# Kernel optimization log

Hardware: AMD Instinct MI355X
Metric: run time of the kernel (lower is better)

Reference implementation:

```python
import jax, jax.numpy as jnp
import numpy as np

HIDDEN = 256
HORIZON = 24
FMET = 16
OUT = 1
EPS = 1e-5


def setup_inputs() -> dict:
    key = jax.random.key(0)
    ks = jax.random.split(key, 12)
    B, N = 16, 1000
    final_h = jax.random.normal(ks[0], (B, N, HIDDEN), dtype=jnp.float32)
    future_met = jax.random.normal(ks[1], (B, HORIZON, N, FMET), dtype=jnp.float32)
    # step_queries: xavier_uniform over (max_horizon, hidden)
    lim_q = float(np.sqrt(6.0 / (HORIZON + HIDDEN)))
    step_queries = jax.random.uniform(ks[2], (HORIZON, HIDDEN), minval=-lim_q, maxval=lim_q, dtype=jnp.float32)
    # future_met_proj: Linear(FMET -> HIDDEN); store weight as (FMET, HIDDEN)
    lim_fm = float(np.sqrt(1.0 / FMET))
    W_fm = jax.random.uniform(ks[3], (FMET, HIDDEN), minval=-lim_fm, maxval=lim_fm, dtype=jnp.float32)
    b_fm = jax.random.uniform(ks[4], (HIDDEN,), minval=-lim_fm, maxval=lim_fm, dtype=jnp.float32)
    gamma = jnp.ones((HIDDEN,), dtype=jnp.float32)
    beta = jnp.zeros((HIDDEN,), dtype=jnp.float32)
    lim1 = float(np.sqrt(1.0 / HIDDEN))
    W1 = jax.random.uniform(ks[5], (HIDDEN, HIDDEN), minval=-lim1, maxval=lim1, dtype=jnp.float32)
    b1 = jax.random.uniform(ks[6], (HIDDEN,), minval=-lim1, maxval=lim1, dtype=jnp.float32)
    W2 = jax.random.uniform(ks[7], (HIDDEN, OUT), minval=-lim1, maxval=lim1, dtype=jnp.float32)
    b2 = jax.random.uniform(ks[8], (OUT,), minval=-lim1, maxval=lim1, dtype=jnp.float32)
    return {
        "final_h": final_h,
        "future_met": future_met,
        "step_queries": step_queries,
        "W_fm": W_fm,
        "b_fm": b_fm,
        "gamma": gamma,
        "beta": beta,
        "W1": W1,
        "b1": b1,
        "W2": W2,
        "b2": b2,
    }


def _layer_norm(x, gamma, beta):
    mu = jnp.mean(x, axis=-1, keepdims=True)
    var = jnp.mean(jnp.square(x - mu), axis=-1, keepdims=True)
    return (x - mu) * jax.lax.rsqrt(var + EPS) * gamma + beta


def reference(final_h, future_met, step_queries, W_fm, b_fm, gamma, beta, W1, b1, W2, b2):
    # final_h: (B, N, H); future_met: (B, T, N, F)
    # combined: (B, N, T, H) = broadcast(final_h) + queries + proj(future_met)
    combined = final_h[:, :, None, :] + step_queries[None, None, :, :]
    fm = jnp.transpose(future_met, (0, 2, 1, 3))  # (B, N, T, F)
    combined = combined + (jnp.einsum("bntf,fh->bnth", fm, W_fm) + b_fm)
    x = _layer_norm(combined, gamma, beta)
    x = jax.nn.gelu(x @ W1 + b1, approximate=False)
    # dropout is identity in eval mode
    out = x @ W2 + b2  # (B, N, T, OUT)
    return jnp.transpose(out, (0, 2, 1, 3))  # (B, T, N, OUT)
```

## Files before the change

### kernel.cpp

```cpp
#include <hip/hip_runtime.h>
#include <hip/hip_bf16.h>
#include <stdint.h>

#define MROWS 32
#define LDA   264
#define FMS   40

typedef __bf16 bf16x8 __attribute__((ext_vector_type(8)));
typedef float  f32x4  __attribute__((ext_vector_type(4)));

__device__ __forceinline__ unsigned short f2bf(float f) {
    union { float f; uint32_t u; } v; v.f = f;
    return (unsigned short)((v.u + 0x7FFFu + ((v.u >> 16) & 1u)) >> 16);
}

__device__ __forceinline__ ushort2 pk_bf16(float a, float b) {
    union { __hip_bfloat162 v; ushort2 u; } c;
    c.v = __float22bfloat162_rn(make_float2(a, b));
    return c.u;
}

__device__ __forceinline__ float gelu_fast(float v) {
    const float t = v * v;
    const float p = fmaf(0.044715f, t, 1.0f);
    const float u = v * p;
    const float e = __builtin_amdgcn_exp2f(u * -2.3021131160186336f);
    return v * __builtin_amdgcn_rcpf(1.0f + e);
}

__global__ __launch_bounds__(256) void prep(const float* __restrict__ W1,
                                            const float* __restrict__ step_q,
                                            const float* __restrict__ b_fm,
                                            const float* __restrict__ W_fm,
                                            unsigned short* __restrict__ w1frag,
                                            float* __restrict__ sqb,
                                            unsigned short* __restrict__ wfmfrag) {
    const int blk = blockIdx.x, tid = threadIdx.x;
    if (blk < 256) {
        const int o  = blk * 256 + tid;
        const int e  = o & 7;
        const int l  = (o >> 3) & 63;
        const int fr = o >> 9;
        const int kk = fr & 7, j = (fr >> 3) & 3, w = fr >> 5;
        const int col = l & 15, qr = l >> 4;
        const int n = (w << 6) + (j << 4) + col;
        const int k = (kk << 5) + (qr << 3) + e;
        w1frag[o] = f2bf(W1[(k << 8) + n]);
    } else if (blk == 256) {
        const float bv = b_fm[tid];
        #pragma unroll
        for (int t = 0; t < 24; ++t) sqb[t * 256 + tid] = step_q[t * 256 + tid] + bv;
    } else {
        #pragma unroll
        for (int f = 0; f < 4; ++f) {
            const int fr = (f << 8) + tid;
            const int l = fr & 63, j = (fr >> 6) & 3, w = fr >> 8;
            const int col = l & 15, qr = l >> 4;
            const int n = (w << 6) + (j << 4) + col;
            #pragma unroll
            for (int e = 0; e < 8; ++e) {
                const int k = (qr << 3) + e;
                wfmfrag[(fr << 3) + e] = (k < 16) ? f2bf(W_fm[(k << 8) + n]) : (unsigned short)0;
            }
        }
    }
}

__global__ __launch_bounds__(256, 6) void fused_head(
    const float* __restrict__ final_h, const float* __restrict__ future_met,
    const float* __restrict__ gamma,   const float* __restrict__ beta,
    const float* __restrict__ b1,      const float* __restrict__ W2,
    const float* __restrict__ b2,      const unsigned short* __restrict__ w1frag,
    const float* __restrict__ sqb,     const unsigned short* __restrict__ wfmfrag,
    float* __restrict__ out)
{
    __shared__ __align__(16) unsigned short Abuf[MROWS * LDA];
    __shared__ __align__(16) unsigned short fmA[MROWS * FMS];
    __shared__ float2 red[4][MROWS];
    __shared__ float2 mv[MROWS];
    __shared__ float  part[4][MROWS];

    const int tid = threadIdx.x;
    const int w   = tid >> 6;
    const int l   = tid & 63;
    const int col = l & 15;
    const int qr  = l >> 4;
    const int m0  = blockIdx.x * MROWS;

    if (tid < 128) {
        const int row = tid >> 2, f0 = (tid & 3) << 2;
        const int m  = m0 + row;
        const int bn = m / 24, tt = m - bn * 24;
        const int b  = bn / 1000, n = bn - b * 1000;
        const float4 v = *(const float4*)&future_met[((((b * 24 + tt) * 1000) + n) << 4) + f0];
        ushort2 lo = pk_bf16(v.x, v.y), hi = pk_bf16(v.z, v.w);
        ushort4 o; o.x = lo.x; o.y = lo.y; o.z = hi.x; o.w = hi.y;
        *(ushort4*)&fmA[row * FMS + f0] = o;
    }
    {
        const int row = tid >> 3, k = 16 + ((tid & 7) << 1);
        *(unsigned int*)&fmA[row * FMS + k] = 0u;
    }
    __syncthreads();

    f32x4 acc[2][4];
    #pragma unroll
    for (int i = 0; i < 2; ++i) {
        #pragma unroll
        for (int r = 0; r < 4; ++r) {
            const int m  = (i << 4) + (qr << 2) + r;
            const int mm = m0 + m;
            const int bn = mm / 24, tt = mm - bn * 24;
            const float* fh = final_h + (bn << 8) + (w << 6) + col;
            const float* sb = sqb + (tt << 8) + (w << 6) + col;
            #pragma unroll
            for (int j = 0; j < 4; ++j)
                acc[i][j][r] = fh[j << 4] + sb[j << 4];
        }
    }
    {
        const bf16x8 af0 = *(const bf16x8*)&fmA[col * FMS + (qr << 3)];
        const bf16x8 af1 = *(const bf16x8*)&fmA[(16 + col) * FMS + (qr << 3)];
        const unsigned short* Bwf = wfmfrag + (w << 11) + (l << 3);
        #pragma unroll
        for (int j = 0; j < 4; ++j) {
            const bf16x8 bf = *(const bf16x8*)(Bwf + (j << 9));
            acc[0][j] = __builtin_amdgcn_mfma_f32_16x16x32_bf16(af0, bf, acc[0][j], 0, 0, 0);
            acc[1][j] = __builtin_amdgcn_mfma_f32_16x16x32_bf16(af1, bf, acc[1][j], 0, 0, 0);
        }
    }

    #pragma unroll
    for (int i = 0; i < 2; ++i) {
        #pragma unroll
        for (int r = 0; r < 4; ++r) {
            float s = 0.f, q = 0.f;
            #pragma unroll
            for (int j = 0; j < 4; ++j) { const float v = acc[i][j][r]; s += v; q = fmaf(v, v, q); }
            s += __shfl_xor(s, 1); q += __shfl_xor(q, 1);
            s += __shfl_xor(s, 2); q += __shfl_xor(q, 2);
            s += __shfl_xor(s, 4); q += __shfl_xor(q, 4);
            s += __shfl_xor(s, 8); q += __shfl_xor(q, 8);
            if (col == 0) red[w][(i << 4) + (qr << 2) + r] = make_float2(s, q);
        }
    }
    __syncthreads();
    if (tid < MROWS) {
        const float2 a0 = red[0][tid], a1 = red[1][tid], a2 = red[2][tid], a3 = red[3][tid];
        const float S = a0.x + a1.x + a2.x + a3.x;
        const float Q = a0.y + a1.y + a2.y + a3.y;
        const float mu = S * 0.00390625f;
        const float rstd = rsqrtf(Q * 0.00390625f - mu * mu + 1e-5f);
        mv[tid] = make_float2(mu, rstd);
    }
    __syncthreads();

    #pragma unroll
    for (int i = 0; i < 2; ++i) {
        #pragma unroll
        for (int r = 0; r < 4; ++r) {
            const int m = (i << 4) + (qr << 2) + r;
            const float2 p = mv[m];
            float vj[4];
            #pragma unroll
            for (int j = 0; j < 4; ++j) {
                const int n = (w << 6) + (j << 4) + col;
                const float s1 = p.y * gamma[n];
                const float s2 = fmaf(-p.x, s1, beta[n]);
                vj[j] = fmaf(acc[i][j][r], s1, s2);
            }
            const ushort2 p01 = pk_bf16(vj[0], vj[1]);
            const ushort2 p23 = pk_bf16(vj[2], vj[3]);
            unsigned short* Ab = &Abuf[m * LDA + (w << 6) + col];
            Ab[0]  = p01.x; Ab[16] = p01.y;
            Ab[32] = p23.x; Ab[48] = p23.y;
        }
    }
    __syncthreads();

    #pragma unroll
    for (int i = 0; i < 2; ++i)
        #pragma unroll
        for (int j = 0; j < 4; ++j)
            acc[i][j] = (f32x4){0.f, 0.f, 0.f, 0.f};

    {
        const unsigned short* Bw  = w1frag + (w << 14) + (l << 3);
        const unsigned short* Ab0 = &Abuf[col * LDA + (qr << 3)];
        const unsigned short* Ab1 = &Abuf[(16 + col) * LDA + (qr << 3)];
        #pragma unroll
        for (int kk = 0; kk < 8; ++kk) {
            const bf16x8 a0 = *(const bf16x8*)(Ab0 + (kk << 5));
            const bf16x8 a1 = *(const bf16x8*)(Ab1 + (kk << 5));
            #pragma unroll
            for (int j = 0; j < 4; ++j) {
                const bf16x8 bf = *(const bf16x8*)(Bw + (j << 12) + (kk << 9));
                acc[0][j] = __builtin_amdgcn_mfma_f32_16x16x32_bf16(a0, bf, acc[0][j], 0, 0, 0);
                acc[1][j] = __builtin_amdgcn_mfma_f32_16x16x32_bf16(a1, bf, acc[1][j], 0, 0, 0);
            }
        }
    }

    {
        float b1v[4], w2v[4];
        #pragma unroll
        for (int j = 0; j < 4; ++j) {
            const int n = (w << 6) + (j << 4) + col;
            b1v[j] = b1[n]; w2v[j] = W2[n];
        }
        #pragma unroll
        for (int i = 0; i < 2; ++i) {
            #pragma unroll
            for (int r = 0; r < 4; ++r) {
                float p = 0.f;
                #pragma unroll
                for (int j = 0; j < 4; ++j) {
                    const float g = gelu_fast(acc[i][j][r] + b1v[j]);
                    p = fmaf(g, w2v[j], p);
                }
                p += __shfl_xor(p, 1);
                p += __shfl_xor(p, 2);
                p += __shfl_xor(p, 4);
                p += __shfl_xor(p, 8);
                if (col == 0) part[w][(i << 4) + (qr << 2) + r] = p;
            }
        }
    }
    __syncthreads();

    if (tid < MROWS) {
        const int m = m0 + tid;
        const float val = part[0][tid] + part[1][tid] + part[2][tid] + part[3][tid] + b2[0];
        const int bn = m / 24, tt = m - bn * 24;
        const int b  = bn / 1000, n = bn - b * 1000;
        out[(b * 24 + tt) * 1000 + n] = val;
    }
}

extern "C" void kernel_launch(void* const* d_in, const int* in_sizes, int n_in,
                              void* d_out, int out_size, void* d_ws, size_t ws_size,
                              hipStream_t stream) {
    const float* final_h    = (const float*)d_in[0];
    const float* future_met = (const float*)d_in[1];
    const float* step_q     = (const float*)d_in[2];
    const float* W_fm       = (const float*)d_in[3];
    const float* b_fm       = (const float*)d_in[4];
    const float* gamma      = (const float*)d_in[5];
    const float* beta       = (const float*)d_in[6];
    const float* W1         = (const float*)d_in[7];
    const float* b1         = (const float*)d_in[8];
    const float* W2         = (const float*)d_in[9];
    const float* b2         = (const float*)d_in[10];

    unsigned short* w1frag  = (unsigned short*)d_ws;
    float*          sqb     = (float*)((char*)d_ws + 131072);
    unsigned short* wfmfrag = (unsigned short*)((char*)d_ws + 155648);
    float* out = (float*)d_out;

    prep<<<258, 256, 0, stream>>>(W1, step_q, b_fm, W_fm, w1frag, sqb, wfmfrag);
    fused_head<<<12000, 256, 0, stream>>>(final_h, future_met, gamma, beta, b1, W2, b2,
                                          w1frag, sqb, wfmfrag, out);
}
```

Baseline: 229.5 us.

## Fold LayerNorm mean/rstd past W1 GEMM and restructure prep weight packing

Moves the LayerNorm normalization after the W1 matmul: the A tile is written as x*gamma in bf16 immediately, and mean/rstd are applied to the GEMM output using precomputed gamma·W1 and beta·W1+b1 vectors. This removes one block barrier and a separate normalize pass before the GEMM. The prep kernel now packs W1 through shared memory with 9 blocks and computes the folded vectors, and the row index math avoids per-row divisions. Feeding un-centered values to bf16 can lose precision when the row mean is large compared with its spread.

```diff
diff --git a/kernel.cpp b/kernel.cpp
--- a/kernel.cpp
+++ b/kernel.cpp
@@ -32,46 +32,63 @@
                                             const float* __restrict__ step_q,
                                             const float* __restrict__ b_fm,
                                             const float* __restrict__ W_fm,
+                                            const float* __restrict__ gamma,
+                                            const float* __restrict__ beta,
+                                            const float* __restrict__ b1,
                                             unsigned short* __restrict__ w1frag,
                                             float* __restrict__ sqb,
-                                            unsigned short* __restrict__ wfmfrag) {
+                                            unsigned short* __restrict__ wfmfrag,
+                                            float* __restrict__ gw1,
+                                            float* __restrict__ b1t) {
     const int blk = blockIdx.x, tid = threadIdx.x;
-    if (blk < 256) {
-        const int o  = blk * 256 + tid;
-        const int e  = o & 7;
-        const int l  = (o >> 3) & 63;
-        const int fr = o >> 9;
-        const int kk = fr & 7, j = (fr >> 3) & 3, w = fr >> 5;
-        const int col = l & 15, qr = l >> 4;
-        const int n = (w << 6) + (j << 4) + col;
-        const int k = (kk << 5) + (qr << 3) + e;
-        w1frag[o] = f2bf(W1[(k << 8) + n]);
-    } else if (blk == 256) {
+    if (blk < 8) {
+        __shared__ unsigned short T[256][40];
+        const int kk = blk;
+        #pragma unroll
+        for (int r = 0; r < 32; ++r)
+            T[tid][r] = f2bf(W1[((kk << 5) + r) * 256 + tid]);
+        __syncthreads();
+        #pragma unroll
+        for (int f = 0; f < 4; ++f) {
+            const int fi = (f << 8) + tid;
+            const int l = fi & 63, j = (fi >> 6) & 3, w = fi >> 8;
+            const int n = (w << 6) + (j << 4) + (l & 15);
+            const uint4 v = *(const uint4*)&T[n][(l >> 4) << 3];
+            *(uint4*)&w1frag[((w << 5) + (j << 3) + kk) * 512 + (l << 3)] = v;
+        }
+    } else {
         const float bv = b_fm[tid];
         #pragma unroll
         for (int t = 0; t < 24; ++t) sqb[t * 256 + tid] = step_q[t * 256 + tid] + bv;
-    } else {
         #pragma unroll
         for (int f = 0; f < 4; ++f) {
             const int fr = (f << 8) + tid;
             const int l = fr & 63, j = (fr >> 6) & 3, w = fr >> 8;
-            const int col = l & 15, qr = l >> 4;
-            const int n = (w << 6) + (j << 4) + col;
+            const int n = (w << 6) + (j << 4) + (l & 15);
+            const int qr = l >> 4;
             #pragma unroll
             for (int e = 0; e < 8; ++e) {
                 const int k = (qr << 3) + e;
                 wfmfrag[(fr << 3) + e] = (k < 16) ? f2bf(W_fm[(k << 8) + n]) : (unsigned short)0;
             }
         }
+        float sg = 0.f, sb = 0.f;
+        for (int k = 0; k < 256; ++k) {
+            const float wv = W1[(k << 8) + tid];
+            sg = fmaf(gamma[k], wv, sg);
+            sb = fmaf(beta[k],  wv, sb);
+        }
+        gw1[tid] = sg;
+        b1t[tid] = sb + b1[tid];
     }
 }
 
 __global__ __launch_bounds__(256, 6) void fused_head(
     const float* __restrict__ final_h, const float* __restrict__ future_met,
-    const float* __restrict__ gamma,   const float* __restrict__ beta,
-    const float* __restrict__ b1,      const float* __restrict__ W2,
+    const float* __restrict__ gamma,   const float* __restrict__ W2,
     const float* __restrict__ b2,      const unsigned short* __restrict__ w1frag,
     const float* __restrict__ sqb,     const unsigned short* __restrict__ wfmfrag,
+    const float* __restrict__ gw1,     const float* __restrict__ b1t,
     float* __restrict__ out)
 {
     __shared__ __align__(16) unsigned short Abuf[MROWS * LDA];
@@ -86,12 +103,16 @@
     const int col = l & 15;
     const int qr  = l >> 4;
     const int m0  = blockIdx.x * MROWS;
+    const int bn0 = m0 / 24;
+    const int tt0 = m0 - bn0 * 24;
 
     if (tid < 128) {
         const int row = tid >> 2, f0 = (tid & 3) << 2;
-        const int m  = m0 + row;
-        const int bn = m / 24, tt = m - bn * 24;
-        const int b  = bn / 1000, n = bn - b * 1000;
+        const int tta = tt0 + row;
+        const int sub = (tta >= 24) + (tta >= 48);
+        const int tt  = tta - sub * 24;
+        const int bn  = bn0 + sub;
+        const int b   = bn / 1000, n = bn - b * 1000;
         const float4 v = *(const float4*)&future_met[((((b * 24 + tt) * 1000) + n) << 4) + f0];
         ushort2 lo = pk_bf16(v.x, v.y), hi = pk_bf16(v.z, v.w);
         ushort4 o; o.x = lo.x; o.y = lo.y; o.z = hi.x; o.w = hi.y;
@@ -103,14 +124,20 @@
     }
     __syncthreads();
 
+    float g_[4];
+    #pragma unroll
+    for (int j = 0; j < 4; ++j) g_[j] = gamma[(w << 6) + (j << 4) + col];
+
     f32x4 acc[2][4];
     #pragma unroll
     for (int i = 0; i < 2; ++i) {
         #pragma unroll
         for (int r = 0; r < 4; ++r) {
-            const int m  = (i << 4) + (qr << 2) + r;
-            const int mm = m0 + m;
-            const int bn = mm / 24, tt = mm - bn * 24;
+            const int d   = (i << 4) + (qr << 2) + r;
+            const int tta = tt0 + d;
+            const int sub = (tta >= 24) + (tta >= 48);
+            const int tt  = tta - sub * 24;
+            const int bn  = bn0 + sub;
             const float* fh = final_h + (bn << 8) + (w << 6) + col;
             const float* sb = sqb + (tt << 8) + (w << 6) + col;
             #pragma unroll
@@ -134,17 +161,28 @@
     for (int i = 0; i < 2; ++i) {
         #pragma unroll
         for (int r = 0; r < 4; ++r) {
-            float s = 0.f, q = 0.f;
-            #pragma unroll
-            for (int j = 0; j < 4; ++j) { const float v = acc[i][j][r]; s += v; q = fmaf(v, v, q); }
+            const int m = (i << 4) + (qr << 2) + r;
+            float s = 0.f, q = 0.f, vj[4];
+            #pragma unroll
+            for (int j = 0; j < 4; ++j) {
+                const float v = acc[i][j][r];
+                s += v; q = fmaf(v, v, q);
+                vj[j] = v * g_[j];
+            }
             s += __shfl_xor(s, 1); q += __shfl_xor(q, 1);
             s += __shfl_xor(s, 2); q += __shfl_xor(q, 2);
             s += __shfl_xor(s, 4); q += __shfl_xor(q, 4);
             s += __shfl_xor(s, 8); q += __shfl_xor(q, 8);
-            if (col == 0) red[w][(i << 4) + (qr << 2) + r] = make_float2(s, q);
-        }
-    }
-    __syncthreads();
+            if (col == 0) red[w][m] = make_float2(s, q);
+            const ushort2 p01 = pk_bf16(vj[0], vj[1]);
+            const ushort2 p23 = pk_bf16(vj[2], vj[3]);
+            unsigned short* Ab = &Abuf[m * LDA + (w << 6) + col];
+            Ab[0]  = p01.x; Ab[16] = p01.y;
+            Ab[32] = p23.x; Ab[48] = p23.y;
+        }
+    }
+    __syncthreads();
+
     if (tid < MROWS) {
         const float2 a0 = red[0][tid], a1 = red[1][tid], a2 = red[2][tid], a3 = red[3][tid];
         const float S = a0.x + a1.x + a2.x + a3.x;
@@ -153,30 +191,6 @@
         const float rstd = rsqrtf(Q * 0.00390625f - mu * mu + 1e-5f);
         mv[tid] = make_float2(mu, rstd);
     }
-    __syncthreads();
-
-    #pragma unroll
-    for (int i = 0; i < 2; ++i) {
-        #pragma unroll
-        for (int r = 0; r < 4; ++r) {
-            const int m = (i << 4) + (qr << 2) + r;
-            const float2 p = mv[m];
-            float vj[4];
-            #pragma unroll
-            for (int j = 0; j < 4; ++j) {
-                const int n = (w << 6) + (j << 4) + col;
-                const float s1 = p.y * gamma[n];
-                const float s2 = fmaf(-p.x, s1, beta[n]);
-                vj[j] = fmaf(acc[i][j][r], s1, s2);
-            }
-            const ushort2 p01 = pk_bf16(vj[0], vj[1]);
-            const ushort2 p23 = pk_bf16(vj[2], vj[3]);
-            unsigned short* Ab = &Abuf[m * LDA + (w << 6) + col];
-            Ab[0]  = p01.x; Ab[16] = p01.y;
-            Ab[32] = p23.x; Ab[48] = p23.y;
-        }
-    }
-    __syncthreads();
 
     #pragma unroll
     for (int i = 0; i < 2; ++i)
@@ -201,29 +215,33 @@
         }
     }
 
-    {
-        float b1v[4], w2v[4];
-        #pragma unroll
-        for (int j = 0; j < 4; ++j) {
-            const int n = (w << 6) + (j << 4) + col;
-            b1v[j] = b1[n]; w2v[j] = W2[n];
-        }
-        #pragma unroll
-        for (int i = 0; i < 2; ++i) {
-            #pragma unroll
-            for (int r = 0; r < 4; ++r) {
-                float p = 0.f;
-                #pragma unroll
-                for (int j = 0; j < 4; ++j) {
-                    const float g = gelu_fast(acc[i][j][r] + b1v[j]);
-                    p = fmaf(g, w2v[j], p);
-                }
-                p += __shfl_xor(p, 1);
-                p += __shfl_xor(p, 2);
-                p += __shfl_xor(p, 4);
-                p += __shfl_xor(p, 8);
-                if (col == 0) part[w][(i << 4) + (qr << 2) + r] = p;
-            }
+    float gwv[4], btv[4], w2v[4];
+    #pragma unroll
+    for (int j = 0; j < 4; ++j) {
+        const int n = (w << 6) + (j << 4) + col;
+        gwv[j] = gw1[n]; btv[j] = b1t[n]; w2v[j] = W2[n];
+    }
+    __syncthreads();
+
+    #pragma unroll
+    for (int i = 0; i < 2; ++i) {
+        #pragma unroll
+        for (int r = 0; r < 4; ++r) {
+            const int m = (i << 4) + (qr << 2) + r;
+            const float2 p = mv[m];
+            const float cm = -p.x * p.y;
+            float pp = 0.f;
+            #pragma unroll
+            for (int j = 0; j < 4; ++j) {
+                const float yv = fmaf(p.y, acc[i][j][r], fmaf(cm, gwv[j], btv[j]));
+                const float g = gelu_fast(yv);
+                pp = fmaf(g, w2v[j], pp);
+            }
+            pp += __shfl_xor(pp, 1);
+            pp += __shfl_xor(pp, 2);
+            pp += __shfl_xor(pp, 4);
+            pp += __shfl_xor(pp, 8);
+            if (col == 0) part[w][m] = pp;
         }
     }
     __syncthreads();
@@ -255,9 +273,12 @@
     unsigned short* w1frag  = (unsigned short*)d_ws;
     float*          sqb     = (float*)((char*)d_ws + 131072);
     unsigned short* wfmfrag = (unsigned short*)((char*)d_ws + 155648);
+    float*          gw1     = (float*)((char*)d_ws + 188416);
+    float*          b1t     = (float*)((char*)d_ws + 189440);
     float* out = (float*)d_out;
 
-    prep<<<258, 256, 0, stream>>>(W1, step_q, b_fm, W_fm, w1frag, sqb, wfmfrag);
-    fused_head<<<12000, 256, 0, stream>>>(final_h, future_met, gamma, beta, b1, W2, b2,
-                                          w1frag, sqb, wfmfrag, out);
-}
+    prep<<<9, 256, 0, stream>>>(W1, step_q, b_fm, W_fm, gamma, beta, b1,
+                                w1frag, sqb, wfmfrag, gw1, b1t);
+    fused_head<<<12000, 256, 0, stream>>>(final_h, future_met, gamma, W2, b2,
+                                          w1frag, sqb, wfmfrag, gw1, b1t, out);
+}
```

Measured after the change: 244.0 us. 6.3% more time.
